# Optimization experiments

Hardware: AMD Instinct MI355X
Metric: run time of the kernel (lower is better)

Reference implementation:

```python
import jax, jax.numpy as jnp
import numpy as np

N_BINS = 15


def setup_inputs() -> dict:
    key = jax.random.key(0)
    k1, k2 = jax.random.split(key)
    N, C = 2000000, 64
    probabilities = jax.random.uniform(k1, (N, C), dtype=jnp.float32)
    labels = jax.random.randint(k2, (N,), 0, C, dtype=jnp.int64)
    return {"probabilities": probabilities, "labels": labels}


def reference(probabilities, labels):
    # confidences/predictions over class dim
    confidences = jnp.max(probabilities, axis=1)
    predictions = jnp.argmax(probabilities, axis=1)
    accuracies = (predictions == labels).astype(confidences.dtype)

    boundaries = jnp.linspace(0.0, 1.0, N_BINS + 1)
    # torch loop uses (lower, upper] bins; digitize(right=True) gives index i
    # s.t. boundaries[i-1] < x <= boundaries[i]. conf == 0 falls in no bin.
    bin_idx = jnp.clip(jnp.digitize(confidences, boundaries, right=True) - 1, 0, N_BINS - 1)
    valid = (confidences > 0).astype(confidences.dtype)

    sum_conf = jax.ops.segment_sum(confidences * valid, bin_idx, num_segments=N_BINS)
    sum_acc = jax.ops.segment_sum(accuracies * valid, bin_idx, num_segments=N_BINS)
    count = jax.ops.segment_sum(valid, bin_idx, num_segments=N_BINS)

    n = confidences.shape[0]
    prop_in_bin = count / n
    safe = jnp.maximum(count, 1.0)
    avg_conf = sum_conf / safe
    avg_acc = sum_acc / safe
    per_bin = jnp.where(count > 0, jnp.abs(avg_conf - avg_acc) * prop_in_bin, 0.0)
    ece = jnp.sum(per_bin)
    return ece.reshape(1)
```

## Files before the change

kernel.cpp:

```cpp
#include <hip/hip_runtime.h>
#include <hip/hip_bf16.h>

#define N_BINS 15
#define C_DIM 64


__global__ __launch_bounds__(256) void ece_main(const float* __restrict__ probs,
                                                const int* __restrict__ labels,
                                                float* __restrict__ gbins, int N) {
    __shared__ float s_bins[3 * N_BINS];
    const int tid = threadIdx.x;
    if (tid < 3 * N_BINS) s_bins[tid] = 0.f;
    __syncthreads();

    const int lane = tid & 63;
    const int wave = tid >> 6;
    const int l4   = lane & 3;
    const int rsub = lane >> 2;
    const int wavesPerBlock = blockDim.x >> 6;

    float c14 = 0.f, a14 = 0.f, n14 = 0.f;
    float c13 = 0.f, a13 = 0.f, n13 = 0.f;

    const long long totalWaves = (long long)gridDim.x * wavesPerBlock;
    long long rowBase = ((long long)blockIdx.x * wavesPerBlock + wave) * 16;
    const long long rstride = totalWaves * 16;

    for (; rowBase < (long long)N; rowBase += rstride) {
        const long long row = rowBase + rsub;
        const bool valid = row < (long long)N;

        float4 v0, v1, v2, v3;
        int lab = 0;
        if (valid) {
            const float* p = probs + row * 64 + l4 * 4;
            v0 = *(const float4*)(p);
            v1 = *(const float4*)(p + 16);
            v2 = *(const float4*)(p + 32);
            v3 = *(const float4*)(p + 48);
            if (l4 == 0) lab = labels[row];
        } else {
            v0 = v1 = v2 = v3 = make_float4(-1.f, -1.f, -1.f, -1.f);
        }

        float m;
        int a;
        {
            const int b0 = l4 * 4;
            m = v0.x; a = b0;
            if (v0.y > m) { m = v0.y; a = b0 + 1; }
            if (v0.z > m) { m = v0.z; a = b0 + 2; }
            if (v0.w > m) { m = v0.w; a = b0 + 3; }
            const int b1 = 16 + b0;
            if (v1.x > m) { m = v1.x; a = b1; }
            if (v1.y > m) { m = v1.y; a = b1 + 1; }
            if (v1.z > m) { m = v1.z; a = b1 + 2; }
            if (v1.w > m) { m = v1.w; a = b1 + 3; }
            const int b2 = 32 + b0;
            if (v2.x > m) { m = v2.x; a = b2; }
            if (v2.y > m) { m = v2.y; a = b2 + 1; }
            if (v2.z > m) { m = v2.z; a = b2 + 2; }
            if (v2.w > m) { m = v2.w; a = b2 + 3; }
            const int b3 = 48 + b0;
            if (v3.x > m) { m = v3.x; a = b3; }
            if (v3.y > m) { m = v3.y; a = b3 + 1; }
            if (v3.z > m) { m = v3.z; a = b3 + 2; }
            if (v3.w > m) { m = v3.w; a = b3 + 3; }
        }

        float conf = valid ? m : -1.f;
        int   pred = a;
        {
            float om = __shfl_xor(conf, 1, 64);
            int   oa = __shfl_xor(pred, 1, 64);
            if (om > conf || (om == conf && oa < pred)) { conf = om; pred = oa; }
            om = __shfl_xor(conf, 2, 64);
            oa = __shfl_xor(pred, 2, 64);
            if (om > conf || (om == conf && oa < pred)) { conf = om; pred = oa; }
        }

        if (l4 == 0 && valid && conf > 0.f) {
            const float acc = (pred == lab) ? 1.f : 0.f;
            int bin = (int)ceilf(conf * 15.f) - 1;
            bin = min(max(bin, 0), N_BINS - 1);
            if (bin == 14)      { c14 += conf; a14 += acc; n14 += 1.f; }
            else if (bin == 13) { c13 += conf; a13 += acc; n13 += 1.f; }
            else {
                atomicAdd(&s_bins[bin],              conf);
                atomicAdd(&s_bins[N_BINS + bin],     acc);
                atomicAdd(&s_bins[2 * N_BINS + bin], 1.f);
            }
        }
    }

    #pragma unroll
    for (int off = 4; off <= 32; off <<= 1) {
        c14 += __shfl_xor(c14, off, 64);
        a14 += __shfl_xor(a14, off, 64);
        n14 += __shfl_xor(n14, off, 64);
        c13 += __shfl_xor(c13, off, 64);
        a13 += __shfl_xor(a13, off, 64);
        n13 += __shfl_xor(n13, off, 64);
    }
    if (lane == 0) {
        atomicAdd(&s_bins[14],              c14);
        atomicAdd(&s_bins[N_BINS + 14],     a14);
        atomicAdd(&s_bins[2 * N_BINS + 14], n14);
        atomicAdd(&s_bins[13],              c13);
        atomicAdd(&s_bins[N_BINS + 13],     a13);
        atomicAdd(&s_bins[2 * N_BINS + 13], n13);
    }
    __syncthreads();
    if (tid < 3 * N_BINS && s_bins[tid] != 0.f) atomicAdd(&gbins[tid], s_bins[tid]);
}

__global__ void ece_final(const float* __restrict__ gbins,
                          float* __restrict__ out, int N) {
    if (threadIdx.x == 0 && blockIdx.x == 0) {
        float ece = 0.f;
        const float invN = 1.f / (float)N;
        for (int b = 0; b < N_BINS; b++) {
            const float sc = gbins[b];
            const float sa = gbins[N_BINS + b];
            const float cn = gbins[2 * N_BINS + b];
            if (cn > 0.f) {
                const float avg_conf = sc / cn;
                const float avg_acc  = sa / cn;
                ece += fabsf(avg_conf - avg_acc) * (cn * invN);
            }
        }
        out[0] = ece;
    }
}

extern "C" void kernel_launch(void* const* d_in, const int* in_sizes, int n_in,
                              void* d_out, int out_size, void* d_ws, size_t ws_size,
                              hipStream_t stream) {
    const float* probs  = (const float*)d_in[0];
    const int*   labels = (const int*)d_in[1];
    float* gbins = (float*)d_ws;
    float* out   = (float*)d_out;

    const int N = in_sizes[1];

    hipMemsetAsync(d_ws, 0, 3 * N_BINS * sizeof(float), stream);

    const int threads = 256;
    const int blocks  = 2048;
    ece_main<<<blocks, threads, 0, stream>>>(probs, labels, gbins, N);
    ece_final<<<1, 64, 0, stream>>>(gbins, out, N);
}
```

Measured before the change: 652.8 us.

## Replace argmax with label-value compare and process two rows per lane group

Drops the per-element argmax index tracking. Accuracy now comes from checking whether the probability at the label index equals the row maximum, so only max values need to be reduced across lanes. Each lane group now loads two rows per iteration using nontemporal 128-bit loads and 32-bit address arithmetic, which raises the number of memory requests in flight. The risk is a semantic change on ties: when several classes share the maximum, the label counts as correct even if argmax would pick an earlier index.

```diff
diff --git a/kernel.cpp b/kernel.cpp
--- a/kernel.cpp
+++ b/kernel.cpp
@@ -1,8 +1,12 @@
 #include <hip/hip_runtime.h>
-#include <hip/hip_bf16.h>
 
 #define N_BINS 15
-#define C_DIM 64
+
+typedef float f32x4 __attribute__((ext_vector_type(4)));
+
+__device__ __forceinline__ f32x4 ntld(const void* p) {
+    return __builtin_nontemporal_load((const f32x4*)p);
+}
 
 
 __global__ __launch_bounds__(256) void ece_main(const float* __restrict__ probs,
@@ -22,65 +26,37 @@
     float c14 = 0.f, a14 = 0.f, n14 = 0.f;
     float c13 = 0.f, a13 = 0.f, n13 = 0.f;
 
-    const long long totalWaves = (long long)gridDim.x * wavesPerBlock;
-    long long rowBase = ((long long)blockIdx.x * wavesPerBlock + wave) * 16;
-    const long long rstride = totalWaves * 16;
+    const unsigned Nu = (unsigned)N;
+    const unsigned totalWaves = (unsigned)gridDim.x * wavesPerBlock;
+    const unsigned stride = totalWaves * 32u;
+    unsigned rbase = ((unsigned)blockIdx.x * wavesPerBlock + wave) * 32u;
+    const char* pb = (const char*)probs;
 
-    for (; rowBase < (long long)N; rowBase += rstride) {
-        const long long row = rowBase + rsub;
-        const bool valid = row < (long long)N;
+    auto doGroup = [&](f32x4 v0, f32x4 v1, f32x4 v2, f32x4 v3, int lab, bool valid) {
+        const float m0 = fmaxf(fmaxf(v0.x, v0.y), fmaxf(v0.z, v0.w));
+        const float m1 = fmaxf(fmaxf(v1.x, v1.y), fmaxf(v1.z, v1.w));
+        const float m2 = fmaxf(fmaxf(v2.x, v2.y), fmaxf(v2.z, v2.w));
+        const float m3 = fmaxf(fmaxf(v3.x, v3.y), fmaxf(v3.z, v3.w));
+        const float m  = fmaxf(fmaxf(m0, m1), fmaxf(m2, m3));
 
-        float4 v0, v1, v2, v3;
-        int lab = 0;
-        if (valid) {
-            const float* p = probs + row * 64 + l4 * 4;
-            v0 = *(const float4*)(p);
-            v1 = *(const float4*)(p + 16);
-            v2 = *(const float4*)(p + 32);
-            v3 = *(const float4*)(p + 48);
-            if (l4 == 0) lab = labels[row];
-        } else {
-            v0 = v1 = v2 = v3 = make_float4(-1.f, -1.f, -1.f, -1.f);
-        }
-
-        float m;
-        int a;
-        {
-            const int b0 = l4 * 4;
-            m = v0.x; a = b0;
-            if (v0.y > m) { m = v0.y; a = b0 + 1; }
-            if (v0.z > m) { m = v0.z; a = b0 + 2; }
-            if (v0.w > m) { m = v0.w; a = b0 + 3; }
-            const int b1 = 16 + b0;
-            if (v1.x > m) { m = v1.x; a = b1; }
-            if (v1.y > m) { m = v1.y; a = b1 + 1; }
-            if (v1.z > m) { m = v1.z; a = b1 + 2; }
-            if (v1.w > m) { m = v1.w; a = b1 + 3; }
-            const int b2 = 32 + b0;
-            if (v2.x > m) { m = v2.x; a = b2; }
-            if (v2.y > m) { m = v2.y; a = b2 + 1; }
-            if (v2.z > m) { m = v2.z; a = b2 + 2; }
-            if (v2.w > m) { m = v2.w; a = b2 + 3; }
-            const int b3 = 48 + b0;
-            if (v3.x > m) { m = v3.x; a = b3; }
-            if (v3.y > m) { m = v3.y; a = b3 + 1; }
-            if (v3.z > m) { m = v3.z; a = b3 + 2; }
-            if (v3.w > m) { m = v3.w; a = b3 + 3; }
-        }
+        const int c2 = (lab >> 4) & 3;
+        const int k2 = lab & 3;
+        const int ow = (lab >> 2) & 3;
+        const f32x4 cc = (c2 & 2) ? ((c2 & 1) ? v3 : v2) : ((c2 & 1) ? v1 : v0);
+        const float e = (k2 & 2) ? ((k2 & 1) ? cc.w : cc.z)
+                                 : ((k2 & 1) ? cc.y : cc.x);
 
         float conf = valid ? m : -1.f;
-        int   pred = a;
-        {
-            float om = __shfl_xor(conf, 1, 64);
-            int   oa = __shfl_xor(pred, 1, 64);
-            if (om > conf || (om == conf && oa < pred)) { conf = om; pred = oa; }
-            om = __shfl_xor(conf, 2, 64);
-            oa = __shfl_xor(pred, 2, 64);
-            if (om > conf || (om == conf && oa < pred)) { conf = om; pred = oa; }
+        float lv   = (valid && ow == l4) ? e : -1.f;
+
+        #pragma unroll
+        for (int off = 1; off <= 2; off <<= 1) {
+            conf = fmaxf(conf, __shfl_xor(conf, off, 64));
+            lv   = fmaxf(lv,   __shfl_xor(lv,   off, 64));
         }
 
         if (l4 == 0 && valid && conf > 0.f) {
-            const float acc = (pred == lab) ? 1.f : 0.f;
+            const float acc = (lv == conf) ? 1.f : 0.f;
             int bin = (int)ceilf(conf * 15.f) - 1;
             bin = min(max(bin, 0), N_BINS - 1);
             if (bin == 14)      { c14 += conf; a14 += acc; n14 += 1.f; }
@@ -91,6 +67,32 @@
                 atomicAdd(&s_bins[2 * N_BINS + bin], 1.f);
             }
         }
+    };
+
+    for (; rbase < Nu; rbase += stride) {
+        const unsigned rowA = rbase + rsub;
+        const unsigned rowB = rowA + 16u;
+        const bool vA = rowA < Nu;
+        const bool vB = rowB < Nu;
+        const unsigned rAc = vA ? rowA : (Nu - 1u);
+        const unsigned rBc = vB ? rowB : (Nu - 1u);
+
+        const char* pA = pb + (rAc * 256u + (unsigned)l4 * 16u);
+        const char* pB = pb + (rBc * 256u + (unsigned)l4 * 16u);
+
+        const f32x4 a0 = ntld(pA);
+        const f32x4 a1 = ntld(pA + 64);
+        const f32x4 a2 = ntld(pA + 128);
+        const f32x4 a3 = ntld(pA + 192);
+        const f32x4 b0 = ntld(pB);
+        const f32x4 b1 = ntld(pB + 64);
+        const f32x4 b2 = ntld(pB + 128);
+        const f32x4 b3 = ntld(pB + 192);
+        const int labA = labels[rAc];
+        const int labB = labels[rBc];
+
+        doGroup(a0, a1, a2, a3, labA, vA);
+        doGroup(b0, b1, b2, b3, labB, vB);
     }
 
     #pragma unroll
```

New measurement: 642.7 us (median of 2 runs). Within noise of the previous version (-1.5%).
